# Optimization experiments

Measured on AMD Instinct MI355X. Metric: run time of the kernel, lower is better.

Reference implementation:

```python
import jax, jax.numpy as jnp
import numpy as np

L = 401            # cfg.n_anchor_bins
MIN_SEP = 2        # cfg.min_separation_bins
TARGET_ALPHA = 0.85
DIST_W, CTCF_W, COMP_W = 1.0, 0.5, 0.5
RATIO_TARGET = 1.5


def setup_inputs() -> dict:
    key = jax.random.key(0)
    k1, k2, k3 = jax.random.split(key, 3)
    B = 256
    contact_map = jax.random.normal(k1, (B, L, L), dtype=jnp.float32)
    compartment_logits = jax.random.normal(k2, (B, L, 2), dtype=jnp.float32)
    ctcf_orientation = (jax.random.randint(k3, (B, L), 0, 3) - 1).astype(jnp.int32)  # {-1,0,1}
    return {"contact_map": contact_map,
            "compartment_logits": compartment_logits,
            "ctcf_orientation": ctcf_orientation}


def reference(contact_map, compartment_logits, ctcf_orientation):
    B, Ld, _ = contact_map.shape
    dt = contact_map.dtype
    idx = jnp.arange(Ld)
    d = jnp.abs(idx[:, None] - idx[None, :])          # (L, L) int distance bins

    # ---- distance decay loss: one segment-reduce instead of a loop over bins ----
    bins = d.reshape(-1)                               # (L*L,)
    cm_sum = contact_map.sum(0).reshape(-1)            # sum over batch, flattened
    per_bin_sum = jax.ops.segment_sum(cm_sum, bins, num_segments=Ld)
    counts = jax.ops.segment_sum(jnp.ones_like(cm_sum), bins, num_segments=Ld)
    mean_c = per_bin_sum / (counts * B)                # mean contact per distance s
    s_vals = jnp.arange(Ld).astype(dt)
    valid = (idx >= MIN_SEP) & jnp.isfinite(mean_c) & (mean_c > 0)
    w = valid.astype(dt)
    n = w.sum()
    log_d = jnp.log(jnp.maximum(s_vals, 1.0))
    log_p = jnp.log(jnp.where(valid, mean_c, 1.0) + 1e-6)
    n_safe = jnp.maximum(n, 1.0)
    x_mean = (w * log_d).sum() / n_safe
    y_mean = (w * log_p).sum() / n_safe
    num = (w * (log_d - x_mean) * (log_p - y_mean)).sum()
    den = (w * (log_d - x_mean) ** 2).sum() + 1e-8
    slope = num / den
    dist_loss = jnp.where(n >= 5, (slope + TARGET_ALPHA) ** 2, jnp.zeros((), dt))

    # ---- CTCF convergence loss ----
    f = (ctcf_orientation == 1).astype(dt)             # (B, L)
    r = (ctcf_orientation == -1).astype(dt)
    convergent = f[:, :, None] * r[:, None, :]         # (B, L, L)
    any_c = (ctcf_orientation != 0).astype(dt)
    any_pair = any_c[:, :, None] * any_c[:, None, :]
    non_conv = any_pair * (1.0 - convergent)
    nc_sum = non_conv.sum()
    hinge = (jax.nn.relu(contact_map) * non_conv).sum() / (nc_sum + 1e-6)
    ctcf_loss = jnp.where(nc_sum < 1.0, jnp.zeros((), dt), hinge)

    # ---- compartment loss ----
    comp = jnp.argmax(jax.lax.stop_gradient(compartment_logits), axis=-1)  # (B, L)
    same = (comp[:, :, None] == comp[:, None, :]).astype(dt)               # (B, L, L)
    maskf = (d >= MIN_SEP).astype(dt)[None]                                # (1, L, L)
    within = (contact_map * same * maskf).sum() / jnp.maximum((same * maskf).sum(), 1.0)
    between = (contact_map * (1.0 - same) * maskf).sum() / jnp.maximum(((1.0 - same) * maskf).sum(), 1.0)
    ratio = within / (jnp.abs(between) + 1e-6)
    comp_loss = jax.nn.relu(RATIO_TARGET - ratio)

    total = DIST_W * dist_loss + CTCF_W * ctcf_loss + COMP_W * comp_loss
    return jnp.stack([dist_loss, ctcf_loss, comp_loss, total])
```

## Files before the change

kernel.cpp:

```cpp
#include <hip/hip_runtime.h>
#include <cmath>

#define LBINS 401
#define LL 160801
#define MIN_SEP 2
#define PSTRIDE 405
#define UNR 8

#define ACC_HANY  401
#define ACC_HCONV 402
#define ACC_SWM   403
#define ACC_SMM   404
#define ACCD_OFF  416
#define PARTS_OFF 512

__global__ void zero_kernel(double* __restrict__ accd) {
    if (threadIdx.x < 2) accd[threadIdx.x] = 0.0;
}

__global__ __launch_bounds__(128)
void prep_kernel(const float* __restrict__ logits,
                 const int* __restrict__ ctcf,
                 double* __restrict__ accd) {
    int b = blockIdx.x;
    int tid = threadIdx.x;
    int n1 = 0, nf = 0, nr = 0, na = 0, adj = 0;
    const float* lg = logits + (size_t)b * LBINS * 2;
    const int*   ct = ctcf   + (size_t)b * LBINS;
    for (int l = tid; l < LBINS; l += 128) {
        int o = ct[l];
        int ci = (lg[2 * l + 1] > lg[2 * l]) ? 1 : 0;
        n1 += ci; nf += (o == 1); nr += (o == -1); na += (o != 0);
        if (l >= 1) {
            int cp = (lg[2 * (l - 1) + 1] > lg[2 * (l - 1)]) ? 1 : 0;
            adj += (ci == cp);
        }
    }
    #pragma unroll
    for (int off = 32; off > 0; off >>= 1) {
        n1 += __shfl_down(n1, off, 64);
        nf += __shfl_down(nf, off, 64);
        nr += __shfl_down(nr, off, 64);
        na += __shfl_down(na, off, 64);
        adj += __shfl_down(adj, off, 64);
    }
    __shared__ int ired[2][5];
    int w = tid >> 6;
    if ((tid & 63) == 0) {
        ired[w][0] = n1; ired[w][1] = nf; ired[w][2] = nr;
        ired[w][3] = na; ired[w][4] = adj;
    }
    __syncthreads();
    if (tid == 0) {
        int N1 = ired[0][0] + ired[1][0];
        int NF = ired[0][1] + ired[1][1];
        int NR = ired[0][2] + ired[1][2];
        int NA = ired[0][3] + ired[1][3];
        int AD = ired[0][4] + ired[1][4];
        int N0 = LBINS - N1;
        unsafeAtomicAdd(&accd[0], (double)NA * NA - (double)NF * NR);
        unsafeAtomicAdd(&accd[1],
            (double)N0 * N0 + (double)N1 * N1 - (double)LBINS - 2.0 * AD);
    }
}

__global__ __launch_bounds__(256)
void diag_kernel(const float* __restrict__ cm,
                 const float* __restrict__ logits,
                 const int* __restrict__ ctcf,
                 float* __restrict__ parts) {
    int b      = blockIdx.x;
    int ihalf  = blockIdx.y & 1;
    int kgroup = blockIdx.y >> 1;
    int u      = threadIdx.x;
    int k      = kgroup * 256 + u;
    bool active = (k < LBINS);

    __shared__ float4 colm[LBINS];
    __shared__ float4 rowm[LBINS];
    __shared__ float  lb[LBINS];
    __shared__ float  sred[4][4];

    const int*   ct = ctcf   + (size_t)b * LBINS;
    const float* lg = logits + (size_t)b * LBINS * 2;
    for (int t = u; t < LBINS; t += 256) {
        int o = ct[t];
        float any = (o != 0) ? 1.f : 0.f;
        float rev = (o == -1) ? 1.f : 0.f;
        float fwd = (o == 1) ? 1.f : 0.f;
        float cj  = (lg[2 * t + 1] > lg[2 * t]) ? 1.f : 0.f;
        colm[t] = make_float4(any, rev, cj, 0.f);
        rowm[t] = make_float4(any, fwd, 2.f * cj - 1.f, 1.f - cj);
        lb[t] = 0.f;
    }
    __syncthreads();

    int i0 = ihalf ? 201 : 0;
    int ie = ihalf ? LBINS : 201;

    const float* cmb = cm + (size_t)b * LL;
    float HA = 0.f, HC = 0.f;
    float SMk = 0.f, SMw = 0.f, SWk = 0.f, SWw = 0.f;

    if (active) {
        int i = i0;
        for (; i + UNR <= ie; i += UNR) {
            float  cv[UNR], sw[UNR];
            float4 cj4[UNR], rm4[UNR];
            #pragma unroll
            for (int q = 0; q < UNR; ++q) {
                int ii = i + q;
                int j  = ii + k;
                int wrapped = (j >= LBINS);
                int jc = wrapped ? j - LBINS : j;
                cv[q]  = cmb[(size_t)ii * LBINS + jc];
                cj4[q] = colm[jc];
                rm4[q] = rowm[ii];
                sw[q]  = wrapped ? 1.f : 0.f;
            }
            #pragma unroll
            for (int q = 0; q < UNR; ++q) {
                float c  = cv[q];
                float rc = fmaxf(c, 0.f);
                HA = fmaf(rm4[q].x * cj4[q].x, rc, HA);
                HC = fmaf(rm4[q].y * cj4[q].y, rc, HC);
                float same = fmaf(rm4[q].z, cj4[q].z, rm4[q].w);
                float sc = same * c;
                float s = sw[q];
                SWw = fmaf(s, sc, SWw);
                SWk = fmaf(1.f - s, sc, SWk);
                SMw = fmaf(s, c, SMw);
                SMk = fmaf(1.f - s, c, SMk);
            }
        }
        for (; i < ie; ++i) {
            int j  = i + k;
            int wrapped = (j >= LBINS);
            int jc = wrapped ? j - LBINS : j;
            float c = cmb[(size_t)i * LBINS + jc];
            float4 cjv = colm[jc];
            float4 rm  = rowm[i];
            float s = wrapped ? 1.f : 0.f;
            float rc = fmaxf(c, 0.f);
            HA = fmaf(rm.x * cjv.x, rc, HA);
            HC = fmaf(rm.y * cjv.y, rc, HC);
            float same = fmaf(rm.z, cjv.z, rm.w);
            float sc = same * c;
            SWw = fmaf(s, sc, SWw);
            SWk = fmaf(1.f - s, sc, SWk);
            SMw = fmaf(s, c, SMw);
            SMk = fmaf(1.f - s, c, SMk);
        }
    }

    float SWm = 0.f, SMm = 0.f;
    if (active) {
        int dw = LBINS - k;
        atomicAdd(&lb[k], SMk);
        if (k > 0) atomicAdd(&lb[dw], SMw);
        float mk = (k >= MIN_SEP) ? 1.f : 0.f;
        float mw = (dw >= MIN_SEP) ? 1.f : 0.f;
        SWm = SWk * mk + SWw * mw;
        SMm = SMk * mk + SMw * mw;
    }

    #pragma unroll
    for (int off = 32; off > 0; off >>= 1) {
        HA  += __shfl_down(HA,  off, 64);
        HC  += __shfl_down(HC,  off, 64);
        SWm += __shfl_down(SWm, off, 64);
        SMm += __shfl_down(SMm, off, 64);
    }
    int w = u >> 6;
    if ((u & 63) == 0) {
        sred[w][0] = HA; sred[w][1] = HC; sred[w][2] = SWm; sred[w][3] = SMm;
    }
    __syncthreads();

    float* pout = parts + (size_t)(blockIdx.y * gridDim.x + blockIdx.x) * PSTRIDE;
    for (int t = u; t < LBINS; t += 256) pout[t] = lb[t];
    if (u == 0) {
        float a = 0.f, c2 = 0.f, s = 0.f, m = 0.f;
        #pragma unroll
        for (int q = 0; q < 4; ++q) {
            a += sred[q][0]; c2 += sred[q][1]; s += sred[q][2]; m += sred[q][3];
        }
        pout[401] = a; pout[402] = c2; pout[403] = s; pout[404] = m;
    }
}

__global__ __launch_bounds__(256)
void reduce_kernel(const float* __restrict__ parts,
                   float* __restrict__ accum, int npart) {
    int s = blockIdx.x;
    int u = threadIdx.x;
    float acc = 0.f;
    for (int p = u; p < npart; p += 256) acc += parts[(size_t)p * PSTRIDE + s];
    #pragma unroll
    for (int off = 32; off > 0; off >>= 1) acc += __shfl_down(acc, off, 64);
    __shared__ float r[4];
    if ((u & 63) == 0) r[u >> 6] = acc;
    __syncthreads();
    if (u == 0) accum[s] = r[0] + r[1] + r[2] + r[3];
}

__device__ double block_reduce_d(double v, double* buf) {
    int tid = threadIdx.x;
    buf[tid] = v;
    __syncthreads();
    for (int off = blockDim.x >> 1; off > 0; off >>= 1) {
        if (tid < off) buf[tid] += buf[tid + off];
        __syncthreads();
    }
    double r = buf[0];
    __syncthreads();
    return r;
}

__global__ __launch_bounds__(512)
void final_kernel(const float* __restrict__ accum,
                  const double* __restrict__ accd,
                  float* __restrict__ out, int B) {
    __shared__ double dred[512];
    int tid = threadIdx.x;

    double nc_sum   = accd[0];
    double same_cnt = accd[1];
    double total_maskf = (double)B * ((double)LL - 3.0 * LBINS + 2.0);
    double diff_cnt = total_maskf - same_cnt;

    float wgt = 0.f, x = 0.f, y = 0.f;
    if (tid < LBINS) {
        float cntB = ((tid == 0) ? (float)LBINS : 2.0f * (float)(LBINS - tid)) * (float)B;
        float mc = accum[tid] / cntB;
        int valid = (tid >= MIN_SEP) && __builtin_isfinite(mc) && (mc > 0.0f);
        wgt = valid ? 1.f : 0.f;
        x = logf(fmaxf((float)tid, 1.0f));
        y = logf((valid ? mc : 1.0f) + 1e-6f);
    }
    double n  = block_reduce_d((double)wgt, dred);
    double Sx = block_reduce_d((double)wgt * x, dred);
    double Sy = block_reduce_d((double)wgt * y, dred);
    double n_safe = fmax(n, 1.0);
    double xm = Sx / n_safe, ym = Sy / n_safe;
    double num = block_reduce_d((double)wgt * ((double)x - xm) * ((double)y - ym), dred);
    double den = block_reduce_d((double)wgt * ((double)x - xm) * ((double)x - xm), dred);

    if (tid == 0) {
        double slope = num / (den + 1e-8);
        float dist_loss = (n >= 5.0) ? (float)((slope + 0.85) * (slope + 0.85)) : 0.0f;

        float ncf = (float)nc_sum;
        float hinge = (accum[ACC_HANY] - accum[ACC_HCONV]) / (ncf + 1e-6f);
        float ctcf_loss = (ncf < 1.0f) ? 0.0f : hinge;

        float SW_m = accum[ACC_SWM];
        float SM_m = accum[ACC_SMM];
        float within  = SW_m / (float)fmax(same_cnt, 1.0);
        float between = (SM_m - SW_m) / (float)fmax(diff_cnt, 1.0);
        float ratio = within / (fabsf(between) + 1e-6f);
        float comp_loss = fmaxf(1.5f - ratio, 0.0f);

        float total = 1.0f * dist_loss + 0.5f * ctcf_loss + 0.5f * comp_loss;
        out[0] = dist_loss;
        out[1] = ctcf_loss;
        out[2] = comp_loss;
        out[3] = total;
    }
}

extern "C" void kernel_launch(void* const* d_in, const int* in_sizes, int n_in,
                              void* d_out, int out_size, void* d_ws, size_t ws_size,
                              hipStream_t stream) {
    const float* cm     = (const float*)d_in[0];
    const float* logits = (const float*)d_in[1];
    const int*   ctcf   = (const int*)d_in[2];
    float* out = (float*)d_out;

    int total = in_sizes[0];
    int B = total / LL;

    float*  wsf   = (float*)d_ws;
    float*  accum = wsf;
    double* accd  = (double*)(wsf + ACCD_OFF);
    float*  parts = wsf + PARTS_OFF;
    int npart = 4 * B;

    zero_kernel<<<1, 64, 0, stream>>>(accd);
    prep_kernel<<<B, 128, 0, stream>>>(logits, ctcf, accd);
    diag_kernel<<<dim3(B, 4), 256, 0, stream>>>(cm, logits, ctcf, parts);
    reduce_kernel<<<PSTRIDE, 256, 0, stream>>>(parts, accum, npart);
    final_kernel<<<1, 512, 0, stream>>>(accum, accd, out, B);
}
```

Measured before the change: 256.8 us.

## Fuse prep/zero/final into main and reduce kernels, pack masks into bytes

Cuts the launch count from five to two. The CTCF and compartment count statistics move into the main diagonal kernel as per-batch integer partials, and the final loss computation is folded into the reduce kernel through a last-block-done atomic counter. The per-bin float4 masks become packed byte bitfields, loaded eight row bytes at a time, and the multiplies become bitmask ANDs, which shrinks shared-memory traffic. The trade-offs are atomic-counter synchronisation and a counter reset inside the main kernel that relies on stream ordering.

After: 253.9 us. No clear change (-1.1%).

```diff
diff --git a/kernel.cpp b/kernel.cpp
--- a/kernel.cpp
+++ b/kernel.cpp
@@ -11,89 +11,77 @@
 #define ACC_HCONV 402
 #define ACC_SWM   403
 #define ACC_SMM   404
-#define ACCD_OFF  416
-#define PARTS_OFF 512
-
-__global__ void zero_kernel(double* __restrict__ accd) {
-    if (threadIdx.x < 2) accd[threadIdx.x] = 0.0;
-}
-
-__global__ __launch_bounds__(128)
-void prep_kernel(const float* __restrict__ logits,
-                 const int* __restrict__ ctcf,
-                 double* __restrict__ accd) {
-    int b = blockIdx.x;
-    int tid = threadIdx.x;
-    int n1 = 0, nf = 0, nr = 0, na = 0, adj = 0;
-    const float* lg = logits + (size_t)b * LBINS * 2;
-    const int*   ct = ctcf   + (size_t)b * LBINS;
-    for (int l = tid; l < LBINS; l += 128) {
-        int o = ct[l];
-        int ci = (lg[2 * l + 1] > lg[2 * l]) ? 1 : 0;
-        n1 += ci; nf += (o == 1); nr += (o == -1); na += (o != 0);
-        if (l >= 1) {
-            int cp = (lg[2 * (l - 1) + 1] > lg[2 * (l - 1)]) ? 1 : 0;
-            adj += (ci == cp);
-        }
-    }
-    #pragma unroll
-    for (int off = 32; off > 0; off >>= 1) {
-        n1 += __shfl_down(n1, off, 64);
-        nf += __shfl_down(nf, off, 64);
-        nr += __shfl_down(nr, off, 64);
-        na += __shfl_down(na, off, 64);
-        adj += __shfl_down(adj, off, 64);
-    }
-    __shared__ int ired[2][5];
-    int w = tid >> 6;
-    if ((tid & 63) == 0) {
-        ired[w][0] = n1; ired[w][1] = nf; ired[w][2] = nr;
-        ired[w][3] = na; ired[w][4] = adj;
-    }
-    __syncthreads();
-    if (tid == 0) {
-        int N1 = ired[0][0] + ired[1][0];
-        int NF = ired[0][1] + ired[1][1];
-        int NR = ired[0][2] + ired[1][2];
-        int NA = ired[0][3] + ired[1][3];
-        int AD = ired[0][4] + ired[1][4];
-        int N0 = LBINS - N1;
-        unsafeAtomicAdd(&accd[0], (double)NA * NA - (double)NF * NR);
-        unsafeAtomicAdd(&accd[1],
-            (double)N0 * N0 + (double)N1 * N1 - (double)LBINS - 2.0 * AD);
-    }
-}
 
 __global__ __launch_bounds__(256)
-void diag_kernel(const float* __restrict__ cm,
+void main_kernel(const float* __restrict__ cm,
                  const float* __restrict__ logits,
                  const int* __restrict__ ctcf,
-                 float* __restrict__ parts) {
+                 float* __restrict__ parts,
+                 int* __restrict__ partsI,
+                 int* __restrict__ cnt) {
     int b      = blockIdx.x;
+    int B      = gridDim.x;
     int ihalf  = blockIdx.y & 1;
     int kgroup = blockIdx.y >> 1;
     int u      = threadIdx.x;
     int k      = kgroup * 256 + u;
     bool active = (k < LBINS);
 
-    __shared__ float4 colm[LBINS];
-    __shared__ float4 rowm[LBINS];
-    __shared__ float  lb[LBINS];
-    __shared__ float  sred[4][4];
+    __shared__ unsigned char colx8[LBINS];
+    __shared__ __align__(8) unsigned char row8[LBINS + 7];
+    __shared__ float lb[LBINS];
+    __shared__ float sred[4][4];
+    __shared__ int   ired[4][4];
 
     const int*   ct = ctcf   + (size_t)b * LBINS;
     const float* lg = logits + (size_t)b * LBINS * 2;
     for (int t = u; t < LBINS; t += 256) {
         int o = ct[t];
-        float any = (o != 0) ? 1.f : 0.f;
-        float rev = (o == -1) ? 1.f : 0.f;
-        float fwd = (o == 1) ? 1.f : 0.f;
-        float cj  = (lg[2 * t + 1] > lg[2 * t]) ? 1.f : 0.f;
-        colm[t] = make_float4(any, rev, cj, 0.f);
-        rowm[t] = make_float4(any, fwd, 2.f * cj - 1.f, 1.f - cj);
+        unsigned any = (o != 0)  ? 1u : 0u;
+        unsigned rev = (o == -1) ? 1u : 0u;
+        unsigned fwd = (o == 1)  ? 1u : 0u;
+        unsigned cj  = (lg[2 * t + 1] > lg[2 * t]) ? 1u : 0u;
+        colx8[t] = (unsigned char)(any | (rev << 1) | (cj << 2));
+        row8[t]  = (unsigned char)(any | (fwd << 1) | ((1u - cj) << 2));
         lb[t] = 0.f;
     }
-    __syncthreads();
+    if (u < 7) row8[LBINS + u] = 0;
+    if (b == 0 && blockIdx.y == 0 && u == 0)
+        __hip_atomic_store(cnt, 0, __ATOMIC_RELAXED, __HIP_MEMORY_SCOPE_AGENT);
+    __syncthreads();
+
+    if (blockIdx.y == 0) {
+        int na = 0, nr = 0, n1 = 0, adj = 0;
+        for (int t = u; t < LBINS; t += 256) {
+            unsigned cb = colx8[t];
+            na += (int)(cb & 1u);
+            nr += (int)((cb >> 1) & 1u);
+            n1 += (int)((cb >> 2) & 1u);
+            if (t >= 1) adj += (int)((((cb ^ colx8[t - 1]) >> 2) & 1u) ^ 1u);
+        }
+        #pragma unroll
+        for (int off = 32; off > 0; off >>= 1) {
+            na  += __shfl_down(na,  off, 64);
+            nr  += __shfl_down(nr,  off, 64);
+            n1  += __shfl_down(n1,  off, 64);
+            adj += __shfl_down(adj, off, 64);
+        }
+        int w = u >> 6;
+        if ((u & 63) == 0) {
+            ired[w][0] = na; ired[w][1] = nr; ired[w][2] = n1; ired[w][3] = adj;
+        }
+        __syncthreads();
+        if (u == 0) {
+            int NA = ired[0][0] + ired[1][0] + ired[2][0] + ired[3][0];
+            int NR = ired[0][1] + ired[1][1] + ired[2][1] + ired[3][1];
+            int N1 = ired[0][2] + ired[1][2] + ired[2][2] + ired[3][2];
+            int AD = ired[0][3] + ired[1][3] + ired[2][3] + ired[3][3];
+            int NF = NA - NR;
+            int N0 = LBINS - N1;
+            partsI[b]     = NA * NA - NF * NR;
+            partsI[B + b] = N0 * N0 + N1 * N1 - LBINS - 2 * AD;
+        }
+    }
 
     int i0 = ihalf ? 201 : 0;
     int ie = ihalf ? LBINS : 201;
@@ -103,54 +91,65 @@
     float SMk = 0.f, SMw = 0.f, SWk = 0.f, SWw = 0.f;
 
     if (active) {
-        int i = i0;
+        auto scalar_step = [&](int ii) {
+            int j = ii + k;
+            int wrapped = (j >= LBINS);
+            int jc = wrapped ? j - LBINS : j;
+            float c = cmb[(size_t)ii * LBINS + jc];
+            unsigned cbq = colx8[jc];
+            unsigned rbq = row8[ii];
+            float rc = fmaxf(c, 0.f);
+            unsigned bnd = rbq & cbq;
+            int m0 = (int)(bnd << 31) >> 31;
+            int m1 = (int)(bnd << 30) >> 31;
+            int ms = (int)((rbq ^ cbq) << 29) >> 31;
+            HA += __int_as_float(__float_as_int(rc) & m0);
+            HC += __int_as_float(__float_as_int(rc) & m1);
+            float cs = __int_as_float(__float_as_int(c) & ms);
+            SMw += wrapped ? c   : 0.f;
+            SMk += wrapped ? 0.f : c;
+            SWw += wrapped ? cs  : 0.f;
+            SWk += wrapped ? 0.f : cs;
+        };
+
+        int i  = i0;
+        int iu = i0 + ((8 - (i0 & 7)) & 7);
+        if (iu > ie) iu = ie;
+        for (; i < iu; ++i) scalar_step(i);
         for (; i + UNR <= ie; i += UNR) {
-            float  cv[UNR], sw[UNR];
-            float4 cj4[UNR], rm4[UNR];
+            unsigned long long rwin = *(const unsigned long long*)(row8 + i);
+            float    cv[UNR];
+            unsigned cb[UNR];
+            int      wr[UNR];
             #pragma unroll
             for (int q = 0; q < UNR; ++q) {
                 int ii = i + q;
                 int j  = ii + k;
                 int wrapped = (j >= LBINS);
                 int jc = wrapped ? j - LBINS : j;
-                cv[q]  = cmb[(size_t)ii * LBINS + jc];
-                cj4[q] = colm[jc];
-                rm4[q] = rowm[ii];
-                sw[q]  = wrapped ? 1.f : 0.f;
+                cv[q] = cmb[(size_t)ii * LBINS + jc];
+                cb[q] = colx8[jc];
+                wr[q] = wrapped;
             }
             #pragma unroll
             for (int q = 0; q < UNR; ++q) {
+                unsigned rbq = (unsigned)(rwin >> (8 * q)) & 0xffu;
                 float c  = cv[q];
                 float rc = fmaxf(c, 0.f);
-                HA = fmaf(rm4[q].x * cj4[q].x, rc, HA);
-                HC = fmaf(rm4[q].y * cj4[q].y, rc, HC);
-                float same = fmaf(rm4[q].z, cj4[q].z, rm4[q].w);
-                float sc = same * c;
-                float s = sw[q];
-                SWw = fmaf(s, sc, SWw);
-                SWk = fmaf(1.f - s, sc, SWk);
-                SMw = fmaf(s, c, SMw);
-                SMk = fmaf(1.f - s, c, SMk);
+                unsigned bnd = rbq & cb[q];
+                int m0 = (int)(bnd << 31) >> 31;
+                int m1 = (int)(bnd << 30) >> 31;
+                int ms = (int)((rbq ^ cb[q]) << 29) >> 31;
+                HA += __int_as_float(__float_as_int(rc) & m0);
+                HC += __int_as_float(__float_as_int(rc) & m1);
+                float cs = __int_as_float(__float_as_int(c) & ms);
+                SMw += wr[q] ? c   : 0.f;
+                SMk += wr[q] ? 0.f : c;
+                SWw += wr[q] ? cs  : 0.f;
+                SWk += wr[q] ? 0.f : cs;
             }
         }
-        for (; i < ie; ++i) {
-            int j  = i + k;
-            int wrapped = (j >= LBINS);
-            int jc = wrapped ? j - LBINS : j;
-            float c = cmb[(size_t)i * LBINS + jc];
-            float4 cjv = colm[jc];
-            float4 rm  = rowm[i];
-            float s = wrapped ? 1.f : 0.f;
-            float rc = fmaxf(c, 0.f);
-            HA = fmaf(rm.x * cjv.x, rc, HA);
-            HC = fmaf(rm.y * cjv.y, rc, HC);
-            float same = fmaf(rm.z, cjv.z, rm.w);
-            float sc = same * c;
-            SWw = fmaf(s, sc, SWw);
-            SWk = fmaf(1.f - s, sc, SWk);
-            SMw = fmaf(s, c, SMw);
-            SMk = fmaf(1.f - s, c, SMk);
-        }
+        for (; i < ie; ++i) scalar_step(i);
     }
 
     float SWm = 0.f, SMm = 0.f;
@@ -158,7 +157,7 @@
         int dw = LBINS - k;
         atomicAdd(&lb[k], SMk);
         if (k > 0) atomicAdd(&lb[dw], SMw);
-        float mk = (k >= MIN_SEP) ? 1.f : 0.f;
+        float mk = (k  >= MIN_SEP) ? 1.f : 0.f;
         float mw = (dw >= MIN_SEP) ? 1.f : 0.f;
         SWm = SWk * mk + SWw * mw;
         SMm = SMk * mk + SMw * mw;
@@ -185,79 +184,128 @@
         for (int q = 0; q < 4; ++q) {
             a += sred[q][0]; c2 += sred[q][1]; s += sred[q][2]; m += sred[q][3];
         }
-        pout[401] = a; pout[402] = c2; pout[403] = s; pout[404] = m;
+        pout[ACC_HANY] = a; pout[ACC_HCONV] = c2;
+        pout[ACC_SWM]  = s; pout[ACC_SMM]   = m;
     }
 }
 
+__device__ double br256(double v, double* buf) {
+    int tid = threadIdx.x;
+    buf[tid] = v;
+    __syncthreads();
+    for (int off = 128; off > 0; off >>= 1) {
+        if (tid < off) buf[tid] += buf[tid + off];
+        __syncthreads();
+    }
+    double r = buf[0];
+    __syncthreads();
+    return r;
+}
+
 __global__ __launch_bounds__(256)
-void reduce_kernel(const float* __restrict__ parts,
-                   float* __restrict__ accum, int npart) {
+void reduce_final_kernel(const float* __restrict__ parts,
+                         const int* __restrict__ partsI,
+                         float* __restrict__ accum,
+                         int* __restrict__ accumI,
+                         int* __restrict__ cnt,
+                         float* __restrict__ out,
+                         int B) {
     int s = blockIdx.x;
     int u = threadIdx.x;
-    float acc = 0.f;
-    for (int p = u; p < npart; p += 256) acc += parts[(size_t)p * PSTRIDE + s];
-    #pragma unroll
-    for (int off = 32; off > 0; off >>= 1) acc += __shfl_down(acc, off, 64);
-    __shared__ float r[4];
-    if ((u & 63) == 0) r[u >> 6] = acc;
-    __syncthreads();
-    if (u == 0) accum[s] = r[0] + r[1] + r[2] + r[3];
-}
-
-__device__ double block_reduce_d(double v, double* buf) {
-    int tid = threadIdx.x;
-    buf[tid] = v;
-    __syncthreads();
-    for (int off = blockDim.x >> 1; off > 0; off >>= 1) {
-        if (tid < off) buf[tid] += buf[tid + off];
+    int npart = 4 * B;
+    __shared__ float r4[4];
+    __shared__ int   ri4[4];
+    __shared__ int   lastFlag;
+
+    if (s < PSTRIDE) {
+        float acc = 0.f;
+        for (int p = u; p < npart; p += 256) acc += parts[(size_t)p * PSTRIDE + s];
+        #pragma unroll
+        for (int off = 32; off > 0; off >>= 1) acc += __shfl_down(acc, off, 64);
+        if ((u & 63) == 0) r4[u >> 6] = acc;
         __syncthreads();
-    }
-    double r = buf[0];
-    __syncthreads();
-    return r;
-}
-
-__global__ __launch_bounds__(512)
-void final_kernel(const float* __restrict__ accum,
-                  const double* __restrict__ accd,
-                  float* __restrict__ out, int B) {
-    __shared__ double dred[512];
-    int tid = threadIdx.x;
-
-    double nc_sum   = accd[0];
-    double same_cnt = accd[1];
+        if (u == 0)
+            __hip_atomic_store(&accum[s], r4[0] + r4[1] + r4[2] + r4[3],
+                               __ATOMIC_RELAXED, __HIP_MEMORY_SCOPE_AGENT);
+    } else {
+        int col = s - PSTRIDE;
+        int acc = 0;
+        for (int p = u; p < B; p += 256) acc += partsI[col * B + p];
+        #pragma unroll
+        for (int off = 32; off > 0; off >>= 1) acc += __shfl_down(acc, off, 64);
+        if ((u & 63) == 0) ri4[u >> 6] = acc;
+        __syncthreads();
+        if (u == 0)
+            __hip_atomic_store(&accumI[col], ri4[0] + ri4[1] + ri4[2] + ri4[3],
+                               __ATOMIC_RELAXED, __HIP_MEMORY_SCOPE_AGENT);
+    }
+
+    if (u == 0) {
+        int prev = __hip_atomic_fetch_add(cnt, 1, __ATOMIC_ACQ_REL,
+                                          __HIP_MEMORY_SCOPE_AGENT);
+        lastFlag = (prev == (int)gridDim.x - 1);
+    }
+    __syncthreads();
+    if (!lastFlag) return;
+
+    __shared__ double dred[256];
+
+    double nc_sum   = (double)__hip_atomic_load(&accumI[0], __ATOMIC_RELAXED,
+                                                __HIP_MEMORY_SCOPE_AGENT);
+    double same_cnt = (double)__hip_atomic_load(&accumI[1], __ATOMIC_RELAXED,
+                                                __HIP_MEMORY_SCOPE_AGENT);
     double total_maskf = (double)B * ((double)LL - 3.0 * LBINS + 2.0);
     double diff_cnt = total_maskf - same_cnt;
 
-    float wgt = 0.f, x = 0.f, y = 0.f;
-    if (tid < LBINS) {
-        float cntB = ((tid == 0) ? (float)LBINS : 2.0f * (float)(LBINS - tid)) * (float)B;
-        float mc = accum[tid] / cntB;
-        int valid = (tid >= MIN_SEP) && __builtin_isfinite(mc) && (mc > 0.0f);
-        wgt = valid ? 1.f : 0.f;
-        x = logf(fmaxf((float)tid, 1.0f));
-        y = logf((valid ? mc : 1.0f) + 1e-6f);
-    }
-    double n  = block_reduce_d((double)wgt, dred);
-    double Sx = block_reduce_d((double)wgt * x, dred);
-    double Sy = block_reduce_d((double)wgt * y, dred);
+    float w0 = 0.f, x0 = 0.f, y0 = 0.f;
+    float w1 = 0.f, x1 = 0.f, y1 = 0.f;
+    {
+        int t0 = u;
+        float a0 = __hip_atomic_load(&accum[t0], __ATOMIC_RELAXED,
+                                     __HIP_MEMORY_SCOPE_AGENT);
+        float cntB = ((t0 == 0) ? (float)LBINS : 2.0f * (float)(LBINS - t0)) * (float)B;
+        float mc = a0 / cntB;
+        int valid = (t0 >= MIN_SEP) && __builtin_isfinite(mc) && (mc > 0.0f);
+        w0 = valid ? 1.f : 0.f;
+        x0 = logf(fmaxf((float)t0, 1.0f));
+        y0 = logf((valid ? mc : 1.0f) + 1e-6f);
+    }
+    int t1 = u + 256;
+    if (t1 < LBINS) {
+        float a1 = __hip_atomic_load(&accum[t1], __ATOMIC_RELAXED,
+                                     __HIP_MEMORY_SCOPE_AGENT);
+        float cntB = 2.0f * (float)(LBINS - t1) * (float)B;
+        float mc = a1 / cntB;
+        int valid = __builtin_isfinite(mc) && (mc > 0.0f);
+        w1 = valid ? 1.f : 0.f;
+        x1 = logf((float)t1);
+        y1 = logf((valid ? mc : 1.0f) + 1e-6f);
+    }
+    double n  = br256((double)w0 + (double)w1, dred);
+    double Sx = br256((double)(w0 * x0) + (double)(w1 * x1), dred);
+    double Sy = br256((double)(w0 * y0) + (double)(w1 * y1), dred);
     double n_safe = fmax(n, 1.0);
     double xm = Sx / n_safe, ym = Sy / n_safe;
-    double num = block_reduce_d((double)wgt * ((double)x - xm) * ((double)y - ym), dred);
-    double den = block_reduce_d((double)wgt * ((double)x - xm) * ((double)x - xm), dred);
-
-    if (tid == 0) {
+    double num = br256((double)w0 * ((double)x0 - xm) * ((double)y0 - ym)
+                     + (double)w1 * ((double)x1 - xm) * ((double)y1 - ym), dred);
+    double den = br256((double)w0 * ((double)x0 - xm) * ((double)x0 - xm)
+                     + (double)w1 * ((double)x1 - xm) * ((double)x1 - xm), dred);
+
+    if (u == 0) {
         double slope = num / (den + 1e-8);
         float dist_loss = (n >= 5.0) ? (float)((slope + 0.85) * (slope + 0.85)) : 0.0f;
 
+        float fHA = __hip_atomic_load(&accum[ACC_HANY],  __ATOMIC_RELAXED, __HIP_MEMORY_SCOPE_AGENT);
+        float fHC = __hip_atomic_load(&accum[ACC_HCONV], __ATOMIC_RELAXED, __HIP_MEMORY_SCOPE_AGENT);
+        float fSW = __hip_atomic_load(&accum[ACC_SWM],   __ATOMIC_RELAXED, __HIP_MEMORY_SCOPE_AGENT);
+        float fSM = __hip_atomic_load(&accum[ACC_SMM],   __ATOMIC_RELAXED, __HIP_MEMORY_SCOPE_AGENT);
+
         float ncf = (float)nc_sum;
-        float hinge = (accum[ACC_HANY] - accum[ACC_HCONV]) / (ncf + 1e-6f);
+        float hinge = (fHA - fHC) / (ncf + 1e-6f);
         float ctcf_loss = (ncf < 1.0f) ? 0.0f : hinge;
 
-        float SW_m = accum[ACC_SWM];
-        float SM_m = accum[ACC_SMM];
-        float within  = SW_m / (float)fmax(same_cnt, 1.0);
-        float between = (SM_m - SW_m) / (float)fmax(diff_cnt, 1.0);
+        float within  = fSW / (float)fmax(same_cnt, 1.0);
+        float between = (fSM - fSW) / (float)fmax(diff_cnt, 1.0);
         float ratio = within / (fabsf(between) + 1e-6f);
         float comp_loss = fmaxf(1.5f - ratio, 0.0f);
 
@@ -280,15 +328,15 @@
     int total = in_sizes[0];
     int B = total / LL;
 
-    float*  wsf   = (float*)d_ws;
-    float*  accum = wsf;
-    double* accd  = (double*)(wsf + ACCD_OFF);
-    float*  parts = wsf + PARTS_OFF;
-    int npart = 4 * B;
-
-    zero_kernel<<<1, 64, 0, stream>>>(accd);
-    prep_kernel<<<B, 128, 0, stream>>>(logits, ctcf, accd);
-    diag_kernel<<<dim3(B, 4), 256, 0, stream>>>(cm, logits, ctcf, parts);
-    reduce_kernel<<<PSTRIDE, 256, 0, stream>>>(parts, accum, npart);
-    final_kernel<<<1, 512, 0, stream>>>(accum, accd, out, B);
+    float* wsf    = (float*)d_ws;
+    float* accum  = wsf;
+    int*   accumI = (int*)(wsf + 408);
+    int*   cnt    = (int*)(wsf + 412);
+    int*   partsI = (int*)(wsf + 416);
+    int parts_off = (416 + 2 * B + 255) & ~255;
+    float* parts  = wsf + parts_off;
+
+    main_kernel<<<dim3(B, 4), 256, 0, stream>>>(cm, logits, ctcf, parts, partsI, cnt);
+    reduce_final_kernel<<<PSTRIDE + 2, 256, 0, stream>>>(parts, partsI, accum,
+                                                         accumI, cnt, out, B);
 }
```
